# Kernel tuning notes

Hardware: AMD Instinct MI355X
Metric: run time of the kernel (lower is better)

Reference implementation:

```python
import jax, jax.numpy as jnp
import numpy as np

B = 512            # molecules
M = 24             # atoms per molecule
N = B * M          # total nodes
F = 128            # num_features
NRBF = 20          # num_rbf_features
CUTOFF = 5.0       # cutoff_dist
NUM_ATOM_TYPES = 100


def setup_inputs() -> dict:
    key = jax.random.key(0)
    ks = jax.random.split(key, 8)
    atoms = jax.random.randint(ks[0], (N,), 0, NUM_ATOM_TYPES, dtype=jnp.int64 if jax.config.jax_enable_x64 else jnp.int32)
    # positions in a ~6A box per molecule so many pairs fall under the 5A cutoff
    atom_positions = jax.random.uniform(ks[1], (N, 3), dtype=jnp.float32) * 6.0
    graph_indexes = jnp.repeat(jnp.arange(B), M)
    emb = jax.random.normal(ks[2], (NUM_ATOM_TYPES, F), dtype=jnp.float32)
    W1 = jax.random.normal(ks[3], (F, F), dtype=jnp.float32) / np.sqrt(F)
    b1 = jnp.zeros((F,), dtype=jnp.float32)
    W2 = jax.random.normal(ks[4], (F, 3 * F), dtype=jnp.float32) / np.sqrt(F)
    b2 = jnp.zeros((3 * F,), dtype=jnp.float32)
    Wf = jax.random.normal(ks[5], (NRBF, 3 * F), dtype=jnp.float32) / np.sqrt(NRBF)
    bf = jnp.zeros((3 * F,), dtype=jnp.float32)
    return {"atoms": atoms, "atom_positions": atom_positions, "graph_indexes": graph_indexes,
            "emb": emb, "W1": W1, "b1": b1, "W2": W2, "b2": b2, "Wf": Wf, "bf": bf}


def _painn_forward(atoms, atom_positions, emb, W1, b1, W2, b2, Wf, bf):
    # node embeddings s_i^0 and zero vector features v_i^0
    s = emb[atoms].reshape(B, M, F)                       # [B,M,F]
    v = jnp.zeros((B, M, F, 3), dtype=s.dtype)            # [B,M,F,3]
    pos = atom_positions.reshape(B, M, 3)

    # per-molecule dense neighbor list (same-molecule pairs within cutoff)
    r = pos[:, :, None, :] - pos[:, None, :, :]           # r_ij = pos_i - pos_j  [B,M,M,3]
    d = jnp.linalg.norm(r, axis=-1)                       # [B,M,M]
    mask = (d < CUTOFF) & ~jnp.eye(M, dtype=bool)         # exclude self (d=0 -> RBF div-by-zero)
    d_safe = jnp.where(mask, d, 1.0)

    # RBF: sin(n*pi*d/cutoff)/d, n = 1..20
    n = jnp.arange(1, NRBF + 1, dtype=s.dtype)
    rbf = jnp.sin(n * (jnp.pi / CUTOFF) * d_safe[..., None]) / d_safe[..., None]   # [B,M,M,20]
    Wedge = rbf @ Wf + bf                                 # edge filter  [B,M,M,3F]

    # node MLP phi(s_j): Linear(F,F) -> SiLU -> Linear(F,3F)
    phi = jax.nn.silu(s @ W1 + b1) @ W2 + b2              # [B,M,3F]

    # gather phi over j, modulate by edge filter, mask invalid edges
    msg = Wedge * phi[:, None, :, :] * mask[..., None]    # [B,M,M,3F]
    ds_m, dv_v, dv_r = jnp.split(msg, 3, axis=-1)         # each [B,M,M,F]

    ds = ds_m.sum(axis=2)                                 # scatter-sum over neighbors j -> [B,M,F]
    rhat = r / d_safe[..., None]                          # unit directions
    dv = (jnp.einsum('bijf,bjfc->bifc', dv_v, v)
          + jnp.einsum('bijf,bijc->bifc', dv_r, rhat))    # [B,M,F,3]

    s_new = s + ds
    v_new = v + dv
    return jnp.concatenate([s_new, v_new.reshape(B, M, 3 * F)], axis=-1)  # [B,M,4F]


def reference(atoms, atom_positions, graph_indexes, emb, W1, b1, W2, b2, Wf, bf):
    del graph_indexes  # batch structure is encoded by the fixed [B,M] layout
    return _painn_forward(atoms, atom_positions, emb, W1, b1, W2, b2, Wf, bf)
```

## Files before the change

### kernel.cpp

```cpp
#include <hip/hip_runtime.h>
#include <hip/hip_bf16.h>
#include <math.h>

#define B 512
#define M 24
#define F 128
#define NRBF 20
#define CUTOFF 5.0f


typedef __attribute__((ext_vector_type(8))) short short8;
typedef __attribute__((ext_vector_type(4))) float f32x4;

#define KIDX(g, e) ((((e) >> 2) << 4) + 4 * (g) + ((e) & 3))

__device__ __forceinline__ unsigned f2bf(float x) {
    unsigned u = __builtin_bit_cast(unsigned, x);
    return (u + 0x7FFFu + ((u >> 16) & 1u)) >> 16;
}

__device__ __forceinline__ short8 pack_frag(unsigned u0, unsigned u1,
                                            unsigned u2, unsigned u3) {
    uint4 t = make_uint4(u0, u1, u2, u3);
    return __builtin_bit_cast(short8, t);
}

__device__ __forceinline__ short8 load_wfrag(const float* __restrict__ W, int ld,
                                             int col, int kbase, int kvalid, int g) {
    unsigned u[4];
#pragma unroll
    for (int q = 0; q < 4; ++q) {
        int k0 = kbase + KIDX(g, 2 * q);
        int k1 = kbase + KIDX(g, 2 * q + 1);
        float f0 = (k0 < kvalid) ? W[(size_t)k0 * ld + col] : 0.f;
        float f1 = (k1 < kvalid) ? W[(size_t)k1 * ld + col] : 0.f;
        u[q] = f2bf(f0) | (f2bf(f1) << 16);
    }
    return pack_frag(u[0], u[1], u[2], u[3]);
}

__device__ __forceinline__ short8 load_afrag(const short* sp, int row, int ldsh,
                                             int kbase, int g) {
    const short* p = sp + row * ldsh + kbase + 4 * g;
    uint2 lo = *(const uint2*)(p);
    uint2 hi = *(const uint2*)(p + 16);
    return pack_frag(lo.x, lo.y, hi.x, hi.y);
}

__global__ __launch_bounds__(512, 2) void painn_kernel(
    const int* __restrict__ atoms,
    const float* __restrict__ apos,
    const float* __restrict__ emb,
    const float* __restrict__ W1, const float* __restrict__ b1,
    const float* __restrict__ W2, const float* __restrict__ b2,
    const float* __restrict__ Wf, const float* __restrict__ bf,
    float* __restrict__ out)
{
    __shared__ __attribute__((aligned(16))) short sH[32 * 136];
    __shared__ __attribute__((aligned(16))) float sPhi[32][F][2];
    __shared__ __attribute__((aligned(16))) short sA[8 * 32 * 40];
    __shared__ __attribute__((aligned(16))) float4 sGeo[M * 32];
    __shared__ __attribute__((aligned(16))) float sPos[M][4];

    const int tid  = threadIdx.x;
    const int b    = blockIdx.x;
    const int wid  = tid >> 6;
    const int lane = tid & 63;
    const int g    = lane >> 4;
    const int lrow = lane & 15;
    const int f2   = wid * 16 + lrow;

    for (int idx = tid; idx < M * (F / 4); idx += 512) {
        int node = idx >> 5;
        int f4 = idx & 31;
        int a = atoms[b * M + node];
        float4 v = reinterpret_cast<const float4*>(emb + (size_t)a * F)[f4];
        unsigned u0 = f2bf(v.x) | (f2bf(v.y) << 16);
        unsigned u1 = f2bf(v.z) | (f2bf(v.w) << 16);
        *reinterpret_cast<uint2*>(&sH[node * 136 + f4 * 4]) = make_uint2(u0, u1);
    }
    for (int t = tid; t < 544; t += 512)
        reinterpret_cast<unsigned*>(sH)[24 * 68 + t] = 0u;
    if (tid < M * 3) sPos[tid / 3][tid % 3] = apos[(size_t)b * M * 3 + tid];
    __syncthreads();

    for (int p = tid; p < M * 32; p += 512) {
        int i = p >> 5, j = p & 31;
        float4 g4 = make_float4(0.f, 0.f, 0.f, 0.f);
        if (j < M) {
            float dx = sPos[i][0] - sPos[j][0];
            float dy = sPos[i][1] - sPos[j][1];
            float dz = sPos[i][2] - sPos[j][2];
            float d = sqrtf(dx * dx + dy * dy + dz * dz);
            if (d < CUTOFF && i != j) {
                float inv = 1.0f / d;
                g4 = make_float4(dx * inv, dy * inv, dz * inv, 1.0f);
            }
        }
        sGeo[p] = g4;
    }

    {
        float b1v = b1[f2];
        f32x4 c[2] = {{0.f, 0.f, 0.f, 0.f}, {0.f, 0.f, 0.f, 0.f}};
#pragma unroll
        for (int ks = 0; ks < 4; ++ks) {
            short8 bfrag = load_wfrag(W1, F, f2, ks * 32, 128, g);
            short8 a0 = load_afrag(sH, lrow, 136, ks * 32, g);
            short8 a1 = load_afrag(sH, 16 + lrow, 136, ks * 32, g);
            c[0] = __builtin_amdgcn_mfma_f32_16x16x32_bf16(a0, bfrag, c[0], 0, 0, 0);
            c[1] = __builtin_amdgcn_mfma_f32_16x16x32_bf16(a1, bfrag, c[1], 0, 0, 0);
        }
        __syncthreads();
#pragma unroll
        for (int rt = 0; rt < 2; ++rt)
#pragma unroll
            for (int r = 0; r < 4; ++r) {
                int row = rt * 16 + g * 4 + r;
                float x = c[rt][r] + b1v;
                float h = x / (1.0f + __expf(-x));
                sH[row * 136 + f2] = (short)f2bf(h);
            }
    }
    __syncthreads();

#pragma unroll
    for (int half = 0; half < 2; ++half) {
        int wcol = half ? (256 + f2) : f2;
        float b2v = b2[wcol];
        f32x4 c[2] = {{0.f, 0.f, 0.f, 0.f}, {0.f, 0.f, 0.f, 0.f}};
#pragma unroll
        for (int ks = 0; ks < 4; ++ks) {
            short8 bfrag = load_wfrag(W2, 3 * F, wcol, ks * 32, 128, g);
            short8 a0 = load_afrag(sH, lrow, 136, ks * 32, g);
            short8 a1 = load_afrag(sH, 16 + lrow, 136, ks * 32, g);
            c[0] = __builtin_amdgcn_mfma_f32_16x16x32_bf16(a0, bfrag, c[0], 0, 0, 0);
            c[1] = __builtin_amdgcn_mfma_f32_16x16x32_bf16(a1, bfrag, c[1], 0, 0, 0);
        }
#pragma unroll
        for (int rt = 0; rt < 2; ++rt)
#pragma unroll
            for (int r = 0; r < 4; ++r) {
                int row = rt * 16 + g * 4 + r;
                sPhi[row][f2][half] = c[rt][r] + b2v;
            }
    }
    __syncthreads();

    short8 wfrag0 = load_wfrag(Wf, 3 * F, f2, 0, NRBF, g);
    short8 wfrag2 = load_wfrag(Wf, 3 * F, 256 + f2, 0, NRBF, g);
    const float bf0v = bf[f2];
    const float bf2v = bf[256 + f2];
    const float kth = 3.14159265358979323846f / CUTOFF;

    for (int ic = 0; ic < 3; ++ic) {
        if (tid < 256) {
            int il = tid >> 5, j = tid & 31;
            int i = ic * 8 + il;
            unsigned pk[16];
#pragma unroll
            for (int q = 0; q < 16; ++q) pk[q] = 0u;
            bool valid = false;
            if (j < M && j != i) {
                float dx = sPos[i][0] - sPos[j][0];
                float dy = sPos[i][1] - sPos[j][1];
                float dz = sPos[i][2] - sPos[j][2];
                float d = sqrtf(dx * dx + dy * dy + dz * dz);
                if (d < CUTOFF) {
                    valid = true;
                    float inv = 1.0f / d;
                    float s1, c1;
                    __sincosf(kth * d, &s1, &c1);
                    float cc = 2.0f * c1;
                    float vp = s1 * inv;
                    float vc = cc * s1 * 0.5f * 2.0f * inv;
                    vc = 2.0f * s1 * c1 * inv;
                    pk[0] = f2bf(vp) | (f2bf(vc) << 16);
#pragma unroll
                    for (int q = 1; q < 10; ++q) {
                        float v3 = cc * vc - vp;
                        float v4 = cc * v3 - vc;
                        pk[q] = f2bf(v3) | (f2bf(v4) << 16);
                        vp = v3; vc = v4;
                    }
                }
            }
            (void)valid;
            short* rp = &sA[(il * 32 + j) * 40];
#pragma unroll
            for (int q = 0; q < 8; ++q)
                *reinterpret_cast<uint2*>(rp + q * 4) = make_uint2(pk[2 * q], pk[2 * q + 1]);
        }
        __syncthreads();

        for (int il = 0; il < 8; ++il) {
            const int i = ic * 8 + il;
            float s0 = 0.f, ax = 0.f, ay = 0.f, az = 0.f;
#pragma unroll
            for (int rt = 0; rt < 2; ++rt) {
                short8 afr = load_afrag(sA, il * 32 + rt * 16 + lrow, 40, 0, g);
                f32x4 z4 = {0.f, 0.f, 0.f, 0.f};
                f32x4 c0 = __builtin_amdgcn_mfma_f32_16x16x32_bf16(afr, wfrag0, z4, 0, 0, 0);
                f32x4 c2 = __builtin_amdgcn_mfma_f32_16x16x32_bf16(afr, wfrag2, z4, 0, 0, 0);
#pragma unroll
                for (int r = 0; r < 4; ++r) {
                    int j = rt * 16 + g * 4 + r;
                    float4 ge = sGeo[i * 32 + j];
                    float ph0 = sPhi[j][f2][0];
                    float ph2 = sPhi[j][f2][1];
                    float t0 = fmaf(bf0v, ge.w, c0[r]);
                    s0 = fmaf(t0, ph0, s0);
                    float t2 = fmaf(bf2v, ge.w, c2[r]);
                    float m2 = t2 * ph2;
                    ax = fmaf(m2, ge.x, ax);
                    ay = fmaf(m2, ge.y, ay);
                    az = fmaf(m2, ge.z, az);
                }
            }
            s0 += __shfl_xor(s0, 16); s0 += __shfl_xor(s0, 32);
            ax += __shfl_xor(ax, 16); ax += __shfl_xor(ax, 32);
            ay += __shfl_xor(ay, 16); ay += __shfl_xor(ay, 32);
            az += __shfl_xor(az, 16); az += __shfl_xor(az, 32);
            if (lane < 16) {
                const int node = b * M + i;
                const int a = atoms[node];
                float embv = emb[(size_t)a * F + f2];
                float* o = out + (size_t)node * (4 * F);
                o[f2] = embv + s0;
                o[F + 3 * f2 + 0] = ax;
                o[F + 3 * f2 + 1] = ay;
                o[F + 3 * f2 + 2] = az;
            }
        }
        __syncthreads();
    }
}

extern "C" void kernel_launch(void* const* d_in, const int* in_sizes, int n_in,
                              void* d_out, int out_size, void* d_ws, size_t ws_size,
                              hipStream_t stream) {
    const int*   atoms = (const int*)d_in[0];
    const float* apos  = (const float*)d_in[1];
    const float* emb = (const float*)d_in[3];
    const float* W1  = (const float*)d_in[4];
    const float* b1  = (const float*)d_in[5];
    const float* W2  = (const float*)d_in[6];
    const float* b2  = (const float*)d_in[7];
    const float* Wf  = (const float*)d_in[8];
    const float* bf  = (const float*)d_in[9];
    float* out = (float*)d_out;

    painn_kernel<<<B, 512, 0, stream>>>(atoms, apos, emb, W1, b1, W2, b2, Wf, bf, out);
}
```

Baseline: 37.64 us.

## Fold edge bias into RBF MFMA and hoist phi into registers

Adds a constant-1 RBF column (k=20) and puts the bias bf in the matching row of the Wf fragment, so the MFMA yields the masked edge filter plus bias and the per-edge bias FMAs go away. Loop-invariant phi values are hoisted into registers instead of being reread from LDS for every i. The separate float4 geometry table is replaced by fp16 unit vectors written during the RBF pass, and the sA row stride is padded to 44. This cuts LDS traffic and a geometry pass, at the cost of bf16 rounding on the bias and fp16 precision on the directions.

```diff
diff --git a/kernel.cpp b/kernel.cpp
--- a/kernel.cpp
+++ b/kernel.cpp
@@ -1,5 +1,6 @@
 #include <hip/hip_runtime.h>
 #include <hip/hip_bf16.h>
+#include <hip/hip_fp16.h>
 #include <math.h>
 
 #define B 512
@@ -7,6 +8,7 @@
 #define F 128
 #define NRBF 20
 #define CUTOFF 5.0f
+#define SA_LD 44
 
 
 typedef __attribute__((ext_vector_type(8))) short short8;
@@ -17,6 +19,10 @@
 __device__ __forceinline__ unsigned f2bf(float x) {
     unsigned u = __builtin_bit_cast(unsigned, x);
     return (u + 0x7FFFu + ((u >> 16) & 1u)) >> 16;
+}
+__device__ __forceinline__ unsigned f2h(float x) {
+    __half h = __float2half(x);
+    return (unsigned)__builtin_bit_cast(unsigned short, h);
 }
 
 __device__ __forceinline__ short8 pack_frag(unsigned u0, unsigned u1,
@@ -34,6 +40,23 @@
         int k1 = kbase + KIDX(g, 2 * q + 1);
         float f0 = (k0 < kvalid) ? W[(size_t)k0 * ld + col] : 0.f;
         float f1 = (k1 < kvalid) ? W[(size_t)k1 * ld + col] : 0.f;
+        u[q] = f2bf(f0) | (f2bf(f1) << 16);
+    }
+    return pack_frag(u[0], u[1], u[2], u[3]);
+}
+
+__device__ __forceinline__ short8 load_wffrag(const float* __restrict__ Wf,
+                                              const float* __restrict__ bfv,
+                                              int col, int g) {
+    unsigned u[4];
+#pragma unroll
+    for (int q = 0; q < 4; ++q) {
+        int k0 = KIDX(g, 2 * q);
+        int k1 = KIDX(g, 2 * q + 1);
+        float f0 = (k0 < NRBF) ? Wf[(size_t)k0 * (3 * F) + col]
+                               : (k0 == NRBF ? bfv[col] : 0.f);
+        float f1 = (k1 < NRBF) ? Wf[(size_t)k1 * (3 * F) + col]
+                               : (k1 == NRBF ? bfv[col] : 0.f);
         u[q] = f2bf(f0) | (f2bf(f1) << 16);
     }
     return pack_frag(u[0], u[1], u[2], u[3]);
@@ -58,8 +81,8 @@
 {
     __shared__ __attribute__((aligned(16))) short sH[32 * 136];
     __shared__ __attribute__((aligned(16))) float sPhi[32][F][2];
-    __shared__ __attribute__((aligned(16))) short sA[8 * 32 * 40];
-    __shared__ __attribute__((aligned(16))) float4 sGeo[M * 32];
+    __shared__ __attribute__((aligned(16))) short sA[8 * 32 * SA_LD];
+    __shared__ __attribute__((aligned(16))) short sGeoH[8 * 32 * 4];
     __shared__ __attribute__((aligned(16))) float sPos[M][4];
 
     const int tid  = threadIdx.x;
@@ -84,22 +107,6 @@
     if (tid < M * 3) sPos[tid / 3][tid % 3] = apos[(size_t)b * M * 3 + tid];
     __syncthreads();
 
-    for (int p = tid; p < M * 32; p += 512) {
-        int i = p >> 5, j = p & 31;
-        float4 g4 = make_float4(0.f, 0.f, 0.f, 0.f);
-        if (j < M) {
-            float dx = sPos[i][0] - sPos[j][0];
-            float dy = sPos[i][1] - sPos[j][1];
-            float dz = sPos[i][2] - sPos[j][2];
-            float d = sqrtf(dx * dx + dy * dy + dz * dz);
-            if (d < CUTOFF && i != j) {
-                float inv = 1.0f / d;
-                g4 = make_float4(dx * inv, dy * inv, dz * inv, 1.0f);
-            }
-        }
-        sGeo[p] = g4;
-    }
-
     {
         float b1v = b1[f2];
         f32x4 c[2] = {{0.f, 0.f, 0.f, 0.f}, {0.f, 0.f, 0.f, 0.f}};
@@ -147,11 +154,19 @@
     }
     __syncthreads();
 
-    short8 wfrag0 = load_wfrag(Wf, 3 * F, f2, 0, NRBF, g);
-    short8 wfrag2 = load_wfrag(Wf, 3 * F, 256 + f2, 0, NRBF, g);
-    const float bf0v = bf[f2];
-    const float bf2v = bf[256 + f2];
+    short8 wfrag0 = load_wffrag(Wf, bf, f2, g);
+    short8 wfrag2 = load_wffrag(Wf, bf, 256 + f2, g);
     const float kth = 3.14159265358979323846f / CUTOFF;
+
+    float ph0[8], ph2[8];
+#pragma unroll
+    for (int rt = 0; rt < 2; ++rt)
+#pragma unroll
+        for (int r = 0; r < 4; ++r) {
+            int j = rt * 16 + g * 4 + r;
+            ph0[rt * 4 + r] = sPhi[j][f2][0];
+            ph2[rt * 4 + r] = sPhi[j][f2][1];
+        }
 
     for (int ic = 0; ic < 3; ++ic) {
         if (tid < 256) {
@@ -160,21 +175,19 @@
             unsigned pk[16];
 #pragma unroll
             for (int q = 0; q < 16; ++q) pk[q] = 0u;
-            bool valid = false;
+            unsigned gxy = 0u, gz = 0u;
             if (j < M && j != i) {
                 float dx = sPos[i][0] - sPos[j][0];
                 float dy = sPos[i][1] - sPos[j][1];
                 float dz = sPos[i][2] - sPos[j][2];
                 float d = sqrtf(dx * dx + dy * dy + dz * dz);
                 if (d < CUTOFF) {
-                    valid = true;
                     float inv = 1.0f / d;
                     float s1, c1;
                     __sincosf(kth * d, &s1, &c1);
                     float cc = 2.0f * c1;
                     float vp = s1 * inv;
-                    float vc = cc * s1 * 0.5f * 2.0f * inv;
-                    vc = 2.0f * s1 * c1 * inv;
+                    float vc = 2.0f * s1 * c1 * inv;
                     pk[0] = f2bf(vp) | (f2bf(vc) << 16);
 #pragma unroll
                     for (int q = 1; q < 10; ++q) {
@@ -183,13 +196,16 @@
                         pk[q] = f2bf(v3) | (f2bf(v4) << 16);
                         vp = v3; vc = v4;
                     }
+                    pk[10] = 0x3F80u;
+                    gxy = f2h(dx * inv) | (f2h(dy * inv) << 16);
+                    gz  = f2h(dz * inv);
                 }
             }
-            (void)valid;
-            short* rp = &sA[(il * 32 + j) * 40];
+            short* rp = &sA[(il * 32 + j) * SA_LD];
 #pragma unroll
             for (int q = 0; q < 8; ++q)
                 *reinterpret_cast<uint2*>(rp + q * 4) = make_uint2(pk[2 * q], pk[2 * q + 1]);
+            *reinterpret_cast<uint2*>(&sGeoH[(il * 32 + j) * 4]) = make_uint2(gxy, gz);
         }
         __syncthreads();
 
@@ -198,23 +214,21 @@
             float s0 = 0.f, ax = 0.f, ay = 0.f, az = 0.f;
 #pragma unroll
             for (int rt = 0; rt < 2; ++rt) {
-                short8 afr = load_afrag(sA, il * 32 + rt * 16 + lrow, 40, 0, g);
+                short8 afr = load_afrag(sA, il * 32 + rt * 16 + lrow, SA_LD, 0, g);
                 f32x4 z4 = {0.f, 0.f, 0.f, 0.f};
                 f32x4 c0 = __builtin_amdgcn_mfma_f32_16x16x32_bf16(afr, wfrag0, z4, 0, 0, 0);
                 f32x4 c2 = __builtin_amdgcn_mfma_f32_16x16x32_bf16(afr, wfrag2, z4, 0, 0, 0);
 #pragma unroll
                 for (int r = 0; r < 4; ++r) {
                     int j = rt * 16 + g * 4 + r;
-                    float4 ge = sGeo[i * 32 + j];
-                    float ph0 = sPhi[j][f2][0];
-                    float ph2 = sPhi[j][f2][1];
-                    float t0 = fmaf(bf0v, ge.w, c0[r]);
-                    s0 = fmaf(t0, ph0, s0);
-                    float t2 = fmaf(bf2v, ge.w, c2[r]);
-                    float m2 = t2 * ph2;
-                    ax = fmaf(m2, ge.x, ax);
-                    ay = fmaf(m2, ge.y, ay);
-                    az = fmaf(m2, ge.z, az);
+                    uint2 gw = *reinterpret_cast<const uint2*>(&sGeoH[(il * 32 + j) * 4]);
+                    float2 xy = __half22float2(__builtin_bit_cast(__half2, gw.x));
+                    float gzf = __half2float(__builtin_bit_cast(__half2, gw.y).x);
+                    s0 = fmaf(c0[r], ph0[rt * 4 + r], s0);
+                    float m2 = c2[r] * ph2[rt * 4 + r];
+                    ax = fmaf(m2, xy.x, ax);
+                    ay = fmaf(m2, xy.y, ay);
+                    az = fmaf(m2, gzf, az);
                 }
             }
             s0 += __shfl_xor(s0, 16); s0 += __shfl_xor(s0, 32);
```

After: 36.12 us. 4.0% less time.
